# Kernel optimization log

Hardware: AMD Instinct MI355X
Metric: run time of the kernel (lower is better)

Reference implementation:

```python
import jax, jax.numpy as jnp
import numpy as np

N = 100_000      # nodes
E = 1_600_000    # edges (avg degree 16)
EP = 500_000     # pos/neg decode edges each
IN, H, OUT = 256, 128, 64


def setup_inputs() -> dict:
    key = jax.random.key(0)
    ks = jax.random.split(key, 8)
    x = jax.random.normal(ks[0], (N, IN), dtype=jnp.float32)
    edge_index = jax.random.randint(ks[1], (2, E), 0, N, dtype=jnp.int32)
    pos_edge_index = jax.random.randint(ks[2], (2, EP), 0, N, dtype=jnp.int32)
    neg_edge_index = jax.random.randint(ks[3], (2, EP), 0, N, dtype=jnp.int32)
    W1 = jax.random.normal(ks[4], (IN, H), dtype=jnp.float32) * (1.0 / np.sqrt(IN))
    b1 = jnp.zeros((H,), dtype=jnp.float32)
    W2 = jax.random.normal(ks[5], (H, OUT), dtype=jnp.float32) * (1.0 / np.sqrt(H))
    b2 = jnp.zeros((OUT,), dtype=jnp.float32)
    return dict(x=x, edge_index=edge_index, pos_edge_index=pos_edge_index,
                neg_edge_index=neg_edge_index, W1=W1, b1=b1, W2=W2, b2=b2)


def _gcn_conv(x, src, dst, norm, W, b, n_nodes):
    # PyG GCNConv: linear transform, then normalized scatter-add aggregation
    h = x @ W                              # [N, out]
    msg = h[src] * norm[:, None]           # gather + scale, [E+N, out]
    agg = jax.ops.segment_sum(msg, dst, num_segments=n_nodes)
    return agg + b


def reference(x, edge_index, pos_edge_index, neg_edge_index, W1, b1, W2, b2):
    n = x.shape[0]
    loops = jnp.arange(n, dtype=edge_index.dtype)
    src = jnp.concatenate([edge_index[0], loops])   # add self-loops (GCNConv default)
    dst = jnp.concatenate([edge_index[1], loops])
    # symmetric normalization D^{-1/2} (A+I) D^{-1/2}
    deg = jax.ops.segment_sum(jnp.ones_like(src, dtype=x.dtype), dst, num_segments=n)
    dinv = jnp.where(deg > 0, jax.lax.rsqrt(jnp.maximum(deg, 1e-12)), 0.0)
    norm = dinv[src] * dinv[dst]
    # encode
    h = jax.nn.relu(_gcn_conv(x, src, dst, norm, W1, b1, n))
    z = _gcn_conv(h, src, dst, norm, W2, b2, n)
    # decode: edge score = <z_u, z_v> over pos+neg edges
    ei = jnp.concatenate([pos_edge_index, neg_edge_index], axis=-1)
    return (z[ei[0]] * z[ei[1]]).sum(axis=-1)   # [2*EP]
```

## Files before the change

kernel.cpp:

```cpp
#include <hip/hip_runtime.h>


#define BUK_SHIFT 7
#define BUK_NODES 128

__global__ __launch_bounds__(256) void b_hist_k(const int* __restrict__ dst, int E,
                                                int nbuk, int* __restrict__ bhist) {
  __shared__ int h[1024];
  for (int i = threadIdx.x; i < nbuk; i += 256) h[i] = 0;
  __syncthreads();
  for (int i = blockIdx.x * 256 + threadIdx.x; i < E; i += gridDim.x * 256)
    atomicAdd(&h[dst[i] >> BUK_SHIFT], 1);
  __syncthreads();
  for (int i = threadIdx.x; i < nbuk; i += 256) {
    int c = h[i];
    if (c) atomicAdd(&bhist[i], c);
  }
}

__global__ __launch_bounds__(256) void b_scan_k(const int* __restrict__ bhist,
                                                int nbuk, int* __restrict__ bbase,
                                                int* __restrict__ bcur) {
  __shared__ int arr[256];
  const int t = threadIdx.x;
  const int per = (nbuk + 255) / 256;
  const int start = t * per;
  const int end = min(start + per, nbuk);
  int s = 0;
  for (int i = start; i < end; ++i) s += bhist[i];
  arr[t] = s;
  __syncthreads();
  for (int off = 1; off < 256; off <<= 1) {
    int v = (t >= off) ? arr[t - off] : 0;
    __syncthreads();
    arr[t] += v;
    __syncthreads();
  }
  int run = arr[t] - s;
  for (int i = start; i < end; ++i) {
    bbase[i] = run;
    bcur[i] = run;
    run += bhist[i];
  }
  if (t == 255) bbase[nbuk] = arr[255];
}

__global__ __launch_bounds__(256) void b_scatter_k(const int* __restrict__ src,
                                                   const int* __restrict__ dst, int E,
                                                   int nbuk, int* __restrict__ bcur,
                                                   int* __restrict__ ebuf) {
  __shared__ int lh[1024];
  __shared__ int lc[1024];
  const int base = blockIdx.x * 8192;
  if (base >= E) return;
  const int end = min(base + 8192, E);
  for (int i = threadIdx.x; i < nbuk; i += 256) lh[i] = 0;
  __syncthreads();
  for (int i = base + threadIdx.x; i < end; i += 256)
    atomicAdd(&lh[dst[i] >> BUK_SHIFT], 1);
  __syncthreads();
  for (int i = threadIdx.x; i < nbuk; i += 256) {
    int c = lh[i];
    lc[i] = c ? atomicAdd(&bcur[i], c) : 0;
  }
  __syncthreads();
  for (int i = base + threadIdx.x; i < end; i += 256) {
    int d = dst[i];
    int pos = atomicAdd(&lc[d >> BUK_SHIFT], 1);
    ebuf[pos] = src[i] | ((d & (BUK_NODES - 1)) << 17);
  }
}

__global__ __launch_bounds__(128) void b_build_k(const int* __restrict__ ebuf,
                                                 const int* __restrict__ bbase, int n,
                                                 int nbuk, float* __restrict__ dinv,
                                                 int* __restrict__ rowptr,
                                                 int* __restrict__ csr) {
  __shared__ int cnt[BUK_NODES];
  __shared__ int pre[BUK_NODES];
  __shared__ int cur[BUK_NODES];
  const int b = blockIdx.x, t = threadIdx.x;
  cnt[t] = 0;
  __syncthreads();
  const int beg = bbase[b], end = bbase[b + 1];
  for (int i = beg + t; i < end; i += 128) atomicAdd(&cnt[ebuf[i] >> 17], 1);
  __syncthreads();
  const int c = cnt[t];
  pre[t] = c;
  __syncthreads();
  for (int off = 1; off < 128; off <<= 1) {
    int v = (t >= off) ? pre[t - off] : 0;
    __syncthreads();
    pre[t] += v;
    __syncthreads();
  }
  const int base = beg + pre[t] - c;
  cur[t] = base;
  const int node = (b << BUK_SHIFT) + t;
  if (node < n) {
    rowptr[node] = base;
    dinv[node] = rsqrtf((float)(c + 1));
  }
  if (b == 0 && t == 0) rowptr[n] = bbase[nbuk];
  __syncthreads();
  for (int i = beg + t; i < end; i += 128) {
    int e = ebuf[i];
    int pos = atomicAdd(&cur[e >> 17], 1);
    csr[pos] = e & 0x1FFFF;
  }
}

template <int BM, int BN, int BK, int TM, int TN>
__global__ __launch_bounds__(256) void gemm_tiled(const float* __restrict__ A,
                                                  const float* __restrict__ B,
                                                  float* __restrict__ C,
                                                  const float* __restrict__ rowscale,
                                                  int M, int K, int N) {
  __shared__ float As[BK][BM + 4];
  __shared__ float Bs[BK][BN + 4];
  const int tid = threadIdx.x;
  const int tx = tid % (BN / TN);
  const int ty = tid / (BN / TN);
  const int rowBase = blockIdx.x * BM;

  float acc[TM][TN];
#pragma unroll
  for (int i = 0; i < TM; ++i)
#pragma unroll
    for (int j = 0; j < TN; ++j) acc[i][j] = 0.f;

  for (int k0 = 0; k0 < K; k0 += BK) {
#pragma unroll
    for (int l = 0; l < BM * BK / (4 * 256); ++l) {
      const int idx = tid + l * 256;
      const int arow = idx / (BK / 4);
      const int acol = (idx % (BK / 4)) * 4;
      const int gr = rowBase + arow;
      float4 v;
      if (gr < M)
        v = *reinterpret_cast<const float4*>(&A[(size_t)gr * K + k0 + acol]);
      else
        v = make_float4(0.f, 0.f, 0.f, 0.f);
      As[acol + 0][arow] = v.x;
      As[acol + 1][arow] = v.y;
      As[acol + 2][arow] = v.z;
      As[acol + 3][arow] = v.w;
    }
#pragma unroll
    for (int l = 0; l < BK * BN / (4 * 256); ++l) {
      const int idx = tid + l * 256;
      const int brow = idx / (BN / 4);
      const int bcol4 = (idx % (BN / 4)) * 4;
      *reinterpret_cast<float4*>(&Bs[brow][bcol4]) =
          *reinterpret_cast<const float4*>(&B[(size_t)(k0 + brow) * N + bcol4]);
    }
    __syncthreads();
#pragma unroll
    for (int kk = 0; kk < BK; ++kk) {
      float ra[TM], rb[TN];
#pragma unroll
      for (int i = 0; i < TM; i += 4)
        *reinterpret_cast<float4*>(&ra[i]) =
            *reinterpret_cast<const float4*>(&As[kk][ty * TM + i]);
#pragma unroll
      for (int j = 0; j < TN; j += 4)
        *reinterpret_cast<float4*>(&rb[j]) =
            *reinterpret_cast<const float4*>(&Bs[kk][tx * TN + j]);
#pragma unroll
      for (int i = 0; i < TM; ++i)
#pragma unroll
        for (int j = 0; j < TN; ++j) acc[i][j] += ra[i] * rb[j];
    }
    __syncthreads();
  }
#pragma unroll
  for (int i = 0; i < TM; ++i) {
    const int gr = rowBase + ty * TM + i;
    if (gr < M) {
      const float s = rowscale[gr];
#pragma unroll
      for (int j = 0; j < TN; j += 4) {
        float4 v = {acc[i][j] * s, acc[i][j + 1] * s, acc[i][j + 2] * s,
                    acc[i][j + 3] * s};
        *reinterpret_cast<float4*>(&C[(size_t)gr * N + tx * TN + j]) = v;
      }
    }
  }
}

template <bool RELU>
__global__ __launch_bounds__(256) void agg128_k(const float* __restrict__ g,
                                                const int* __restrict__ rowptr,
                                                const int* __restrict__ csr,
                                                const float* __restrict__ dinv,
                                                const float* __restrict__ bias,
                                                float* __restrict__ hout, int n) {
  const int wid = (blockIdx.x * 256 + threadIdx.x) >> 6;
  if (wid >= n) return;
  const int lane = threadIdx.x & 63;
  const int half = lane >> 5;
  const size_t col = (size_t)(lane & 31) * 4;
  const float dd = dinv[wid];
  const int beg = rowptr[wid];
  const int end = rowptr[wid + 1];
  float4 acc = make_float4(0.f, 0.f, 0.f, 0.f);
  int e = beg;
  for (; e + 8 <= end; e += 8) {
    const int s0 = csr[e + 0 + half];
    const int s1 = csr[e + 2 + half];
    const int s2 = csr[e + 4 + half];
    const int s3 = csr[e + 6 + half];
    const float4 v0 = *reinterpret_cast<const float4*>(&g[(size_t)s0 * 128 + col]);
    const float4 v1 = *reinterpret_cast<const float4*>(&g[(size_t)s1 * 128 + col]);
    const float4 v2 = *reinterpret_cast<const float4*>(&g[(size_t)s2 * 128 + col]);
    const float4 v3 = *reinterpret_cast<const float4*>(&g[(size_t)s3 * 128 + col]);
    acc.x += (v0.x + v1.x) + (v2.x + v3.x);
    acc.y += (v0.y + v1.y) + (v2.y + v3.y);
    acc.z += (v0.z + v1.z) + (v2.z + v3.z);
    acc.w += (v0.w + v1.w) + (v2.w + v3.w);
  }
  for (; e + 2 <= end; e += 2) {
    const int s = csr[e + half];
    const float4 v = *reinterpret_cast<const float4*>(&g[(size_t)s * 128 + col]);
    acc.x += v.x;
    acc.y += v.y;
    acc.z += v.z;
    acc.w += v.w;
  }
  if (e < end && half == 0) {
    const int s = csr[e];
    const float4 v = *reinterpret_cast<const float4*>(&g[(size_t)s * 128 + col]);
    acc.x += v.x;
    acc.y += v.y;
    acc.z += v.z;
    acc.w += v.w;
  }
  acc.x += __shfl_xor(acc.x, 32);
  acc.y += __shfl_xor(acc.y, 32);
  acc.z += __shfl_xor(acc.z, 32);
  acc.w += __shfl_xor(acc.w, 32);
  if (half == 0) {
    const float4 sv = *reinterpret_cast<const float4*>(&g[(size_t)wid * 128 + col]);
    const float4 b = *reinterpret_cast<const float4*>(&bias[col]);
    float4 r;
    r.x = dd * (acc.x + sv.x) + b.x;
    r.y = dd * (acc.y + sv.y) + b.y;
    r.z = dd * (acc.z + sv.z) + b.z;
    r.w = dd * (acc.w + sv.w) + b.w;
    if (RELU) {
      r.x = fmaxf(r.x, 0.f);
      r.y = fmaxf(r.y, 0.f);
      r.z = fmaxf(r.z, 0.f);
      r.w = fmaxf(r.w, 0.f);
    }
    *reinterpret_cast<float4*>(&hout[(size_t)wid * 128 + col]) = r;
  }
}

__global__ __launch_bounds__(256) void agg64_k(const float* __restrict__ g,
                                               const int* __restrict__ rowptr,
                                               const int* __restrict__ csr,
                                               const float* __restrict__ dinv,
                                               const float* __restrict__ bias,
                                               float* __restrict__ hout, int n) {
  const int wid = (blockIdx.x * 256 + threadIdx.x) >> 6;
  if (wid >= n) return;
  const int lane = threadIdx.x & 63;
  const int quad = lane >> 4;
  const size_t col = (size_t)(lane & 15) * 4;
  const float dd = dinv[wid];
  const int beg = rowptr[wid];
  const int end = rowptr[wid + 1];
  float4 acc = make_float4(0.f, 0.f, 0.f, 0.f);
  int e = beg;
  for (; e + 16 <= end; e += 16) {
    const int s0 = csr[e + 0 + quad];
    const int s1 = csr[e + 4 + quad];
    const int s2 = csr[e + 8 + quad];
    const int s3 = csr[e + 12 + quad];
    const float4 v0 = *reinterpret_cast<const float4*>(&g[(size_t)s0 * 64 + col]);
    const float4 v1 = *reinterpret_cast<const float4*>(&g[(size_t)s1 * 64 + col]);
    const float4 v2 = *reinterpret_cast<const float4*>(&g[(size_t)s2 * 64 + col]);
    const float4 v3 = *reinterpret_cast<const float4*>(&g[(size_t)s3 * 64 + col]);
    acc.x += (v0.x + v1.x) + (v2.x + v3.x);
    acc.y += (v0.y + v1.y) + (v2.y + v3.y);
    acc.z += (v0.z + v1.z) + (v2.z + v3.z);
    acc.w += (v0.w + v1.w) + (v2.w + v3.w);
  }
  for (; e + 4 <= end; e += 4) {
    const int s = csr[e + quad];
    const float4 v = *reinterpret_cast<const float4*>(&g[(size_t)s * 64 + col]);
    acc.x += v.x;
    acc.y += v.y;
    acc.z += v.z;
    acc.w += v.w;
  }
  const int r = end - e;
  if (quad < r) {
    const int s = csr[e + quad];
    const float4 v = *reinterpret_cast<const float4*>(&g[(size_t)s * 64 + col]);
    acc.x += v.x;
    acc.y += v.y;
    acc.z += v.z;
    acc.w += v.w;
  }
  acc.x += __shfl_xor(acc.x, 16);
  acc.y += __shfl_xor(acc.y, 16);
  acc.z += __shfl_xor(acc.z, 16);
  acc.w += __shfl_xor(acc.w, 16);
  acc.x += __shfl_xor(acc.x, 32);
  acc.y += __shfl_xor(acc.y, 32);
  acc.z += __shfl_xor(acc.z, 32);
  acc.w += __shfl_xor(acc.w, 32);
  if (quad == 0) {
    const float4 sv = *reinterpret_cast<const float4*>(&g[(size_t)wid * 64 + col]);
    const float4 b = *reinterpret_cast<const float4*>(&bias[col]);
    float4 res;
    res.x = dd * (acc.x + sv.x) + b.x;
    res.y = dd * (acc.y + sv.y) + b.y;
    res.z = dd * (acc.z + sv.z) + b.z;
    res.w = dd * (acc.w + sv.w) + b.w;
    *reinterpret_cast<float4*>(&hout[(size_t)wid * 64 + col]) = res;
  }
}

__global__ __launch_bounds__(256) void decode_k(const int* __restrict__ pos,
                                                const int* __restrict__ neg,
                                                const float* __restrict__ z,
                                                float* __restrict__ out, int EP) {
  const long long t = (long long)blockIdx.x * 256 + threadIdx.x;
  const long long e = t >> 3;
  const int lane = (int)(t & 7);
  if (e >= 2LL * EP) return;
  int u, v;
  if (e < EP) {
    u = pos[e];
    v = pos[EP + e];
  } else {
    u = neg[e - EP];
    v = neg[EP + (e - EP)];
  }
  const float* zu = &z[(size_t)u * 64 + lane * 8];
  const float* zv = &z[(size_t)v * 64 + lane * 8];
  const float4 a0 = *reinterpret_cast<const float4*>(zu);
  const float4 a1 = *reinterpret_cast<const float4*>(zu + 4);
  const float4 b0 = *reinterpret_cast<const float4*>(zv);
  const float4 b1 = *reinterpret_cast<const float4*>(zv + 4);
  float p = a0.x * b0.x + a0.y * b0.y + a0.z * b0.z + a0.w * b0.w +
            a1.x * b1.x + a1.y * b1.y + a1.z * b1.z + a1.w * b1.w;
#pragma unroll
  for (int off = 4; off > 0; off >>= 1) p += __shfl_down(p, off, 8);
  if (lane == 0) out[e] = p;
}


extern "C" void kernel_launch(void* const* d_in, const int* in_sizes, int n_in,
                              void* d_out, int out_size, void* d_ws, size_t ws_size,
                              hipStream_t stream) {
  const float* x = (const float*)d_in[0];
  const int* ei = (const int*)d_in[1];
  const int* pos = (const int*)d_in[2];
  const int* neg = (const int*)d_in[3];
  const float* W1 = (const float*)d_in[4];
  const float* b1 = (const float*)d_in[5];
  const float* W2 = (const float*)d_in[6];
  const float* b2 = (const float*)d_in[7];
  float* out = (float*)d_out;

  const int H = in_sizes[5];
  const int IN = in_sizes[4] / H;
  const int OUT = in_sizes[7];
  const int N = in_sizes[0] / IN;
  const int E = in_sizes[1] / 2;
  const int EP = in_sizes[2] / 2;

  char* ws = (char*)d_ws;
  size_t off = 0;
  auto carve = [&](size_t bytes) -> char* {
    char* p = ws + off;
    off += (bytes + 255) & ~(size_t)255;
    return p;
  };
  const int NBUK = (N + BUK_NODES - 1) >> BUK_SHIFT;

  float* dinvb = (float*)carve((size_t)N * 4);
  int* rowptr = (int*)carve((size_t)(N + 1) * 4);
  int* bhist = (int*)carve((size_t)NBUK * 4);
  int* bbase = (int*)carve((size_t)(NBUK + 1) * 4);
  int* bcur = (int*)carve((size_t)NBUK * 4);
  int* ebuf = (int*)carve((size_t)E * 4);
  int* csr = (int*)carve((size_t)E * 4);
  float* bufA = (float*)carve((size_t)N * H * 4);
  float* bufB = (float*)carve((size_t)N * H * 4);
  (void)ws_size;

  const int* srcp = ei;
  const int* dstp = ei + E;

  hipMemsetAsync(bhist, 0, (size_t)NBUK * 4, stream);
  b_hist_k<<<512, 256, 0, stream>>>(dstp, E, NBUK, bhist);
  b_scan_k<<<1, 256, 0, stream>>>(bhist, NBUK, bbase, bcur);
  b_scatter_k<<<(E + 8191) / 8192, 256, 0, stream>>>(srcp, dstp, E, NBUK, bcur, ebuf);
  b_build_k<<<NBUK, 128, 0, stream>>>(ebuf, bbase, N, NBUK, dinvb, rowptr, csr);

  gemm_tiled<64, 128, 32, 8, 4>
      <<<(N + 63) / 64, 256, 0, stream>>>(x, W1, bufA, dinvb, N, IN, H);
  agg128_k<true><<<(N + 3) / 4, 256, 0, stream>>>(bufA, rowptr, csr, dinvb, b1,
                                                  bufB, N);
  gemm_tiled<64, 64, 32, 4, 4>
      <<<(N + 63) / 64, 256, 0, stream>>>(bufB, W2, bufA, dinvb, N, H, OUT);
  agg64_k<<<(N + 3) / 4, 256, 0, stream>>>(bufA, rowptr, csr, dinvb, b2, bufB, N);
  const long long threads = 2LL * EP * 8;
  decode_k<<<(int)((threads + 255) / 256), 256, 0, stream>>>(pos, neg, bufB, out, EP);
}
```

Baseline: 434.3 us.

## Retile FP32 GEMMs to 128-row blocks with direct global-to-LDS weight loads

```diff
diff --git a/kernel.cpp b/kernel.cpp
--- a/kernel.cpp
+++ b/kernel.cpp
@@ -110,66 +110,74 @@
   }
 }
 
-template <int BM, int BN, int BK, int TM, int TN>
+template <int BN, int NBLK>
 __global__ __launch_bounds__(256) void gemm_tiled(const float* __restrict__ A,
                                                   const float* __restrict__ B,
                                                   float* __restrict__ C,
                                                   const float* __restrict__ rowscale,
-                                                  int M, int K, int N) {
-  __shared__ float As[BK][BM + 4];
-  __shared__ float Bs[BK][BN + 4];
+                                                  int M, int K) {
+  constexpr int BM = 128, BK = 32, TM = 8;
+  __shared__ float As[BK * (BM + 1)];
+  __shared__ float Bs[BK * BN];
   const int tid = threadIdx.x;
-  const int tx = tid % (BN / TN);
-  const int ty = tid / (BN / TN);
+  const int tx = tid & 15;
+  const int ty = tid >> 4;
+  const int lane = tid & 63;
+  const int wave = tid >> 6;
   const int rowBase = blockIdx.x * BM;
 
-  float acc[TM][TN];
+  float acc[TM][NBLK * 4];
 #pragma unroll
   for (int i = 0; i < TM; ++i)
 #pragma unroll
-    for (int j = 0; j < TN; ++j) acc[i][j] = 0.f;
+    for (int j = 0; j < NBLK * 4; ++j) acc[i][j] = 0.f;
+
+  constexpr int BS_BYTES = BK * BN * 4;
+  constexpr int CALLS = BS_BYTES / (4 * 1024);
 
   for (int k0 = 0; k0 < K; k0 += BK) {
-#pragma unroll
-    for (int l = 0; l < BM * BK / (4 * 256); ++l) {
+    {
+      const char* gsrc = (const char*)(B + (size_t)k0 * BN);
+#pragma unroll
+      for (int q = 0; q < CALLS; ++q) {
+        const int off = wave * (CALLS * 1024) + q * 1024 + lane * 16;
+        __builtin_amdgcn_global_load_lds((const __attribute__((address_space(1))) void*)(gsrc + off),
+                                         (__attribute__((address_space(3))) void*)((char*)Bs + off),
+                                         16, 0, 0);
+      }
+    }
+#pragma unroll
+    for (int l = 0; l < 4; ++l) {
       const int idx = tid + l * 256;
-      const int arow = idx / (BK / 4);
-      const int acol = (idx % (BK / 4)) * 4;
+      const int arow = idx >> 3;
+      const int acol = (idx & 7) * 4;
       const int gr = rowBase + arow;
       float4 v;
       if (gr < M)
         v = *reinterpret_cast<const float4*>(&A[(size_t)gr * K + k0 + acol]);
       else
         v = make_float4(0.f, 0.f, 0.f, 0.f);
-      As[acol + 0][arow] = v.x;
-      As[acol + 1][arow] = v.y;
-      As[acol + 2][arow] = v.z;
-      As[acol + 3][arow] = v.w;
+      As[(acol + 0) * (BM + 1) + arow] = v.x;
+      As[(acol + 1) * (BM + 1) + arow] = v.y;
+      As[(acol + 2) * (BM + 1) + arow] = v.z;
+      As[(acol + 3) * (BM + 1) + arow] = v.w;
     }
-#pragma unroll
-    for (int l = 0; l < BK * BN / (4 * 256); ++l) {
-      const int idx = tid + l * 256;
-      const int brow = idx / (BN / 4);
-      const int bcol4 = (idx % (BN / 4)) * 4;
-      *reinterpret_cast<float4*>(&Bs[brow][bcol4]) =
-          *reinterpret_cast<const float4*>(&B[(size_t)(k0 + brow) * N + bcol4]);
-    }
     __syncthreads();
 #pragma unroll
     for (int kk = 0; kk < BK; ++kk) {
-      float ra[TM], rb[TN];
+      float ra[TM], rb[NBLK * 4];
 #pragma unroll
       for (int i = 0; i < TM; i += 4)
         *reinterpret_cast<float4*>(&ra[i]) =
-            *reinterpret_cast<const float4*>(&As[kk][ty * TM + i]);
-#pragma unroll
-      for (int j = 0; j < TN; j += 4)
-        *reinterpret_cast<float4*>(&rb[j]) =
-            *reinterpret_cast<const float4*>(&Bs[kk][tx * TN + j]);
+            *reinterpret_cast<const float4*>(&As[kk * (BM + 1) + ty * TM + i]);
+#pragma unroll
+      for (int b = 0; b < NBLK; ++b)
+        *reinterpret_cast<float4*>(&rb[b * 4]) =
+            *reinterpret_cast<const float4*>(&Bs[kk * BN + b * 64 + tx * 4]);
 #pragma unroll
       for (int i = 0; i < TM; ++i)
 #pragma unroll
-        for (int j = 0; j < TN; ++j) acc[i][j] += ra[i] * rb[j];
+        for (int j = 0; j < NBLK * 4; ++j) acc[i][j] += ra[i] * rb[j];
     }
     __syncthreads();
   }
@@ -179,10 +187,10 @@
     if (gr < M) {
       const float s = rowscale[gr];
 #pragma unroll
-      for (int j = 0; j < TN; j += 4) {
-        float4 v = {acc[i][j] * s, acc[i][j + 1] * s, acc[i][j + 2] * s,
-                    acc[i][j + 3] * s};
-        *reinterpret_cast<float4*>(&C[(size_t)gr * N + tx * TN + j]) = v;
+      for (int b = 0; b < NBLK; ++b) {
+        float4 v = {acc[i][b * 4 + 0] * s, acc[i][b * 4 + 1] * s,
+                    acc[i][b * 4 + 2] * s, acc[i][b * 4 + 3] * s};
+        *reinterpret_cast<float4*>(&C[(size_t)gr * BN + b * 64 + tx * 4]) = v;
       }
     }
   }
@@ -373,6 +381,7 @@
   const int N = in_sizes[0] / IN;
   const int E = in_sizes[1] / 2;
   const int EP = in_sizes[2] / 2;
+  (void)OUT;
 
   char* ws = (char*)d_ws;
   size_t off = 0;
@@ -403,12 +412,12 @@
   b_scatter_k<<<(E + 8191) / 8192, 256, 0, stream>>>(srcp, dstp, E, NBUK, bcur, ebuf);
   b_build_k<<<NBUK, 128, 0, stream>>>(ebuf, bbase, N, NBUK, dinvb, rowptr, csr);
 
-  gemm_tiled<64, 128, 32, 8, 4>
-      <<<(N + 63) / 64, 256, 0, stream>>>(x, W1, bufA, dinvb, N, IN, H);
+  gemm_tiled<128, 2>
+      <<<(N + 127) / 128, 256, 0, stream>>>(x, W1, bufA, dinvb, N, IN);
   agg128_k<true><<<(N + 3) / 4, 256, 0, stream>>>(bufA, rowptr, csr, dinvb, b1,
                                                   bufB, N);
-  gemm_tiled<64, 64, 32, 4, 4>
-      <<<(N + 63) / 64, 256, 0, stream>>>(bufB, W2, bufA, dinvb, N, H, OUT);
+  gemm_tiled<64, 1>
+      <<<(N + 127) / 128, 256, 0, stream>>>(bufB, W2, bufA, dinvb, N, H);
   agg64_k<<<(N + 3) / 4, 256, 0, stream>>>(bufA, rowptr, csr, dinvb, b2, bufB, N);
   const long long threads = 2LL * EP * 8;
   decode_k<<<(int)((threads + 255) / 256), 256, 0, stream>>>(pos, neg, bufB, out, EP);
```

After: 525.9 us. +21.1%, slower.
